# Kernel optimization log

Hardware: AMD Instinct MI355X
Metric: run time of the kernel (lower is better)

The kernel has to match this reference:

```python
import jax, jax.numpy as jnp
import numpy as np

B, N, E = 32, 116, 1346
IN_V, IN_E, H, OUT = 116, 5, 64, 4
NEG_SLOPE = 0.01  # torch LeakyReLU default


def setup_inputs() -> dict:
    key = jax.random.key(0)
    ks = jax.random.split(key, 13)
    return {
        "H_v": jax.random.normal(ks[0], (B * N, IN_V), jnp.float32),
        "H_e": jax.random.normal(ks[1], (B * E, IN_E), jnp.float32),
        "adj_v": jax.random.uniform(ks[2], (B * N, N), jnp.float32),
        "adj_e": jax.random.uniform(ks[3], (B * E, E), jnp.float32),
        "T": jax.random.uniform(ks[4], (B * N, E), jnp.float32),
        "W_v": jax.random.normal(ks[5], (IN_V, H), jnp.float32) * (1.0 / np.sqrt(H)),
        "p_v": jax.random.normal(ks[6], (1, IN_E), jnp.float32),
        "b_v": jax.random.normal(ks[7], (H,), jnp.float32) * 0.01,
        "W_e": jax.random.normal(ks[8], (IN_E, H), jnp.float32) * (1.0 / np.sqrt(H)),
        "p_e": jax.random.normal(ks[9], (1, H), jnp.float32),
        "b_e": jax.random.normal(ks[10], (H,), jnp.float32) * 0.01,
        "W_fc": jax.random.normal(ks[11], (H, OUT), jnp.float32) * (1.0 / np.sqrt(OUT)),
        "b_fc": jax.random.normal(ks[12], (OUT,), jnp.float32) * 0.01,
    }


def _net(H_v, H_e, adj_v, adj_e, T, W_v, p_v, b_v, W_e, p_e, b_e, W_fc, b_fc):
    # reshape flat [B*N, ...] / [B*E, ...] layouts to batched, as in AlternateConvolution.forward
    Hv = H_v.reshape(B, N, IN_V)
    He = H_e.reshape(B, E, IN_E)
    Av = adj_v.reshape(B, N, N)
    Ae = adj_e.reshape(B, E, E)
    Tm = T.reshape(B, N, E)
    eyeN = jnp.eye(N, dtype=bool)
    eyeE = jnp.eye(E, dtype=bool)

    # ---- node layer (AlternateConvolution, node_layer=True) ----
    de = jnp.einsum('bef,f->be', He, p_v[0])                      # H_e @ p^T -> diag values [B,E]
    mult1 = jnp.einsum('bne,be,bme->bnm', Tm, de, Tm)             # T diag(de) T^T
    M1 = jnp.where(eyeN, 1.0, mult1)                              # ones on diagonal
    adjA = M1 * Av
    Hv = jnp.einsum('bnm,bmh->bnh', adjA, Hv @ W_v) + b_v         # [B,N,H]
    Hv = jax.nn.leaky_relu(Hv, NEG_SLOPE)

    # ---- edge layer (AlternateConvolution, node_layer=False) ----
    dv = jnp.einsum('bnh,h->bn', Hv, p_e[0])                      # H_v @ p^T -> diag values [B,N]
    mult2 = jnp.einsum('bne,bn,bnf->bef', Tm, dv, Tm)             # T^T diag(dv) T
    M3 = jnp.where(eyeE, 1.0, mult2)
    adjE = M3 * Ae
    adjE = adjE / (jnp.max(adjE, axis=2, keepdims=True) + 1e-10)  # row-max normalize
    He = jnp.einsum('bef,bfh->beh', adjE, He @ W_e) + b_e         # [B,E,H]
    He = jax.nn.leaky_relu(He, NEG_SLOPE)

    # ---- mean graph pooling over nodes + classifier head (dropout off in eval) ----
    pooled = Hv.mean(axis=1)                                      # [B,H]
    return pooled @ W_fc + b_fc                                   # [B,OUT]


def reference(H_v, H_e, adj_v, adj_e, T, W_v, p_v, b_v, W_e, p_e, b_e, W_fc, b_fc):
    return _net(H_v, H_e, adj_v, adj_e, T, W_v, p_v, b_v, W_e, p_e, b_e, W_fc, b_fc)
```

## Files before the change

kernel.cpp:

```cpp
#include <hip/hip_runtime.h>

#define BATCH 32
#define NN 116
#define EE 1346
#define HH 64
#define SPLITS 8
#define ECH 170
#define MBLK 256
#define HVBLK 116
#define GRID1 (MBLK + HVBLK + 1)

typedef __attribute__((ext_vector_type(8))) short bf16x8;
typedef __attribute__((ext_vector_type(4))) float f32x4;

__device__ __forceinline__ unsigned int cvtpk(float a, float b) {
    unsigned int r;
    asm("v_cvt_pk_bf16_f32 %0, %1, %2" : "=v"(r) : "v"(a), "v"(b));
    return r;
}
__device__ __forceinline__ unsigned short bf16_1(float a) {
    union { float f; unsigned int u; } ua; ua.f = a;
    return (unsigned short)((ua.u + 0x7FFFu + ((ua.u >> 16) & 1u)) >> 16);
}
__device__ __forceinline__ float bf2f(unsigned int bits16) {
    union { unsigned int u; float f; } x; x.u = bits16 << 16;
    return x.f;
}

__global__ __launch_bounds__(512) void stage1_kernel(
    const float* __restrict__ T, const float* __restrict__ He,
    const float* __restrict__ pv,
    const float* __restrict__ Hv, const float* __restrict__ Wv,
    const float* __restrict__ bfc,
    unsigned short* __restrict__ part16, float* __restrict__ HvW,
    float* __restrict__ out)
{
    const int blk = blockIdx.x;
    const int tid = threadIdx.x;

    __shared__ float del[192];
    __shared__ unsigned int Tt[128 * 32];
    __shared__ unsigned int dTt[128 * 32];

    if (blk < MBLK) {
        const int s = blk & 7, b = blk >> 3;
        const int e0 = s * ECH;
        const int cnt = min(ECH, EE - e0);
        const int nsteps = 3;

        {
            const float p0 = pv[0], p1 = pv[1], p2 = pv[2], p3 = pv[3], p4 = pv[4];
            for (int i = tid; i < 192; i += 512) {
                float v = 0.f;
                if (i < cnt) {
                    const float* he = He + (size_t)(b * EE + e0 + i) * 5;
                    v = he[0]*p0 + he[1]*p1 + he[2]*p2 + he[3]*p3 + he[4]*p4;
                }
                del[i] = v;
            }
        }

        const int srow = tid >> 2;
        const int q    = tid & 3;
        const bool rowok = srow < NN;
        const float* Trow = T + ((size_t)b * NN + srow) * EE + e0;

        float2 pf[8];
        auto pref_fast = [&](int c) {
            const int k0 = c * 64 + q * 16;
            #pragma unroll
            for (int j = 0; j < 8; ++j) {
                float2 v = {0.f, 0.f};
                if (rowok) v = *(const float2*)&Trow[k0 + 2 * j];
                pf[j] = v;
            }
        };
        auto pref_chk = [&](int c) {
            const int k0 = c * 64 + q * 16;
            #pragma unroll
            for (int j = 0; j < 8; ++j) {
                float2 v = {0.f, 0.f};
                const int k = k0 + 2 * j;
                if (rowok && k + 1 < cnt) v = *(const float2*)&Trow[k];
                else if (rowok && k < cnt) v.x = Trow[k];
                pf[j] = v;
            }
        };
        auto wlds = [&](int c) {
            const int k0 = c * 64 + q * 16;
            uint4 t0, t1, d0, d1;
            unsigned int* tp0 = &t0.x;  unsigned int* tp1 = &t1.x;
            unsigned int* dp0 = &d0.x;  unsigned int* dp1 = &d1.x;
            #pragma unroll
            for (int j = 0; j < 4; ++j) {
                const float2 va = pf[j];
                const float2 vb = pf[4 + j];
                const float2 da = *(const float2*)&del[k0 + 2 * j];
                const float2 db = *(const float2*)&del[k0 + 8 + 2 * j];
                tp0[j] = cvtpk(va.x, va.y);
                tp1[j] = cvtpk(vb.x, vb.y);
                dp0[j] = cvtpk(va.x * da.x, va.y * da.y);
                dp1[j] = cvtpk(vb.x * db.x, vb.y * db.y);
            }
            const int swz = (srow & 7) << 4;
            const int bo  = srow * 128 + q * 32;
            *(uint4*)((char*)Tt  + ((bo) ^ swz))      = t0;
            *(uint4*)((char*)Tt  + ((bo + 16) ^ swz)) = t1;
            *(uint4*)((char*)dTt + ((bo) ^ swz))      = d0;
            *(uint4*)((char*)dTt + ((bo + 16) ^ swz)) = d1;
        };

        const int w = tid >> 6, lane = tid & 63;
        const int wr = w >> 2, wc = w & 3;
        const int rl = lane & 15, g = lane >> 4;

        auto fragT = [&](const unsigned int* base, int row, int kkb) -> bf16x8 {
            return *(const bf16x8*)((const char*)base + ((row * 128 + kkb + g * 16) ^ ((row & 7) << 4)));
        };

        f32x4 acc[4][2] = {};

        pref_fast(0);
        __syncthreads();

        for (int c = 0; c < nsteps; ++c) {
            wlds(c);
            if (c + 1 == nsteps - 1) pref_fast(c + 1);
            else if (c + 1 < nsteps)  pref_chk(c + 1);
            __syncthreads();
            #pragma unroll
            for (int kk = 0; kk < 2; ++kk) {
                bf16x8 af[4], bf[2];
                #pragma unroll
                for (int i = 0; i < 4; ++i) af[i] = fragT(dTt, wr * 64 + i * 16 + rl, kk * 64);
                #pragma unroll
                for (int j = 0; j < 2; ++j) bf[j] = fragT(Tt,  wc * 32 + j * 16 + rl, kk * 64);
                #pragma unroll
                for (int tn = 0; tn < 4; ++tn)
                    #pragma unroll
                    for (int tm = 0; tm < 2; ++tm)
                        acc[tn][tm] = __builtin_amdgcn_mfma_f32_16x16x32_bf16(
                            af[tn], bf[tm], acc[tn][tm], 0, 0, 0);
            }
            __syncthreads();
        }

        #pragma unroll
        for (int tn = 0; tn < 4; ++tn) {
            #pragma unroll
            for (int r = 0; r < 4; ++r) {
                const int grow = wr * 64 + tn * 16 + g * 4 + r;
                if (grow >= NN) continue;
                unsigned short* rowp = part16 + (((size_t)b * NN + grow) * SPLITS + s) * 128;
                #pragma unroll
                for (int tm = 0; tm < 2; ++tm)
                    rowp[wc * 32 + tm * 16 + rl] = bf16_1(acc[tn][tm][r]);
            }
        }
    } else if (blk < MBLK + HVBLK) {
        const int l0 = (blk - MBLK) * 32 + (tid >> 6) * 4;
        const int h  = tid & 63;
        const float* hv0 = Hv + (size_t)(l0 + 0) * NN;
        const float* hv1 = Hv + (size_t)(l0 + 1) * NN;
        const float* hv2 = Hv + (size_t)(l0 + 2) * NN;
        const float* hv3 = Hv + (size_t)(l0 + 3) * NN;
        float a0 = 0.f, a1 = 0.f, a2 = 0.f, a3 = 0.f;
        #pragma unroll 4
        for (int k = 0; k < NN; ++k) {
            const float wv = Wv[k * HH + h];
            a0 = fmaf(hv0[k], wv, a0);
            a1 = fmaf(hv1[k], wv, a1);
            a2 = fmaf(hv2[k], wv, a2);
            a3 = fmaf(hv3[k], wv, a3);
        }
        HvW[(size_t)(l0 + 0) * HH + h] = a0;
        HvW[(size_t)(l0 + 1) * HH + h] = a1;
        HvW[(size_t)(l0 + 2) * HH + h] = a2;
        HvW[(size_t)(l0 + 3) * HH + h] = a3;
    } else {
        if (tid < BATCH * 4) out[tid] = bfc[tid & 3];
    }
}

__global__ __launch_bounds__(256) void stage2_kernel(
    const unsigned short* __restrict__ part16, const float* __restrict__ Av,
    const float* __restrict__ HvW, const float* __restrict__ bv,
    const float* __restrict__ Wfc, float* __restrict__ out)
{
    const int blk = blockIdx.x;
    const int b = blk >> 3;
    const int n0 = (blk & 7) * 16;
    const int tid = threadIdx.x;
    const int w = tid >> 6, lane = tid & 63;
    const int rl = lane & 15, g = lane >> 4;

    __shared__ unsigned int Cb[4096];
    __shared__ unsigned int Ab[1024];
    __shared__ float sl[64];

    for (int idx = tid; idx < 64 * 64; idx += 256) {
        const int h = idx & 63, np = idx >> 6;
        const int n = 2 * np;
        const float v0 = (n < NN)     ? HvW[((size_t)b * NN + n) * HH + h]     : 0.f;
        const float v1 = (n + 1 < NN) ? HvW[((size_t)b * NN + n + 1) * HH + h] : 0.f;
        *(unsigned int*)((char*)Cb + ((h * 256 + np * 4) ^ ((h & 7) << 4))) = cvtpk(v0, v1);
    }

    {
        const int r = tid >> 4, m0 = (tid & 15) * 8;
        const int n = n0 + r;
        float ms[8] = {0.f,0.f,0.f,0.f,0.f,0.f,0.f,0.f};
        unsigned int outw[4];
        if (n < NN) {
            const unsigned short* pp = part16 + (((size_t)b * NN + n) * SPLITS) * 128 + m0;
            #pragma unroll
            for (int s = 0; s < SPLITS; ++s) {
                const uint4 u = *(const uint4*)(pp + (size_t)s * 128);
                const unsigned int* up = &u.x;
                #pragma unroll
                for (int j = 0; j < 4; ++j) {
                    ms[2*j]   += bf2f(up[j] & 0xffffu);
                    ms[2*j+1] += bf2f(up[j] >> 16);
                }
            }
            const float* avp = Av + ((size_t)b * NN + n) * NN;
            #pragma unroll
            for (int j = 0; j < 4; ++j) {
                const int m = m0 + 2 * j;
                const float a0 = (m < NN)     ? avp[m]     : 0.f;
                const float a1 = (m + 1 < NN) ? avp[m + 1] : 0.f;
                const float v0 = a0 * ((m     == n) ? 1.0f : ms[2*j]);
                const float v1 = a1 * ((m + 1 == n) ? 1.0f : ms[2*j+1]);
                outw[j] = cvtpk(v0, v1);
            }
        } else {
            outw[0] = outw[1] = outw[2] = outw[3] = 0u;
        }
        *(uint4*)((char*)Ab + ((r * 256 + m0 * 2) ^ ((r & 7) << 4))) = *(uint4*)outw;
    }
    __syncthreads();

    f32x4 acc = {};
    #pragma unroll
    for (int kk = 0; kk < 4; ++kk) {
        const int hrow = w * 16 + rl;
        const bf16x8 a  = *(const bf16x8*)((const char*)Ab +
                          ((rl * 256 + kk * 64 + g * 16) ^ ((rl & 7) << 4)));
        const bf16x8 bb = *(const bf16x8*)((const char*)Cb +
                          ((hrow * 256 + kk * 64 + g * 16) ^ ((hrow & 7) << 4)));
        acc = __builtin_amdgcn_mfma_f32_16x16x32_bf16(a, bb, acc, 0, 0, 0);
    }
    {
        const int h = w * 16 + rl;
        const float bias = bv[h];
        float s = 0.f;
        #pragma unroll
        for (int r = 0; r < 4; ++r) {
            const int n = n0 + g * 4 + r;
            if (n < NN) {
                const float x = acc[r] + bias;
                s += (x >= 0.f) ? x : 0.01f * x;
            }
        }
        s += __shfl_xor(s, 16);
        s += __shfl_xor(s, 32);
        if (g == 0) sl[h] = s;
    }
    __syncthreads();

    if (tid < 4) {
        float a = 0.f;
        #pragma unroll 16
        for (int k = 0; k < HH; ++k)
            a = fmaf(sl[k], Wfc[k * 4 + tid], a);
        atomicAdd(&out[b * 4 + tid], a * (1.0f / NN));
    }
}

extern "C" void kernel_launch(void* const* d_in, const int* in_sizes, int n_in,
                              void* d_out, int out_size, void* d_ws, size_t ws_size,
                              hipStream_t stream) {
    const float* Hv  = (const float*)d_in[0];
    const float* He  = (const float*)d_in[1];
    const float* Av  = (const float*)d_in[2];
    const float* T_  = (const float*)d_in[4];
    const float* Wv  = (const float*)d_in[5];
    const float* pv  = (const float*)d_in[6];
    const float* bv  = (const float*)d_in[7];
    const float* Wfc = (const float*)d_in[11];
    const float* bfc = (const float*)d_in[12];
    float* out = (float*)d_out;

    unsigned short* part16 = (unsigned short*)d_ws;
    float* HvW = (float*)(part16 + (size_t)BATCH * NN * SPLITS * 128);

    stage1_kernel<<<GRID1, 512, 0, stream>>>(
        T_, He, pv, Hv, Wv, bfc, part16, HvW, out);
    stage2_kernel<<<BATCH * 8, 256, 0, stream>>>(
        part16, Av, HvW, bv, Wfc, out);
}
```

Before: 31.95 us.

## Prefetch all T chunks up front and fold HvW GEMV into MFMA blocks

New measurement: 38.78 us. 1.21x slower.

```diff
diff --git a/kernel.cpp b/kernel.cpp
--- a/kernel.cpp
+++ b/kernel.cpp
@@ -7,8 +7,6 @@
 #define SPLITS 8
 #define ECH 170
 #define MBLK 256
-#define HVBLK 116
-#define GRID1 (MBLK + HVBLK + 1)
 
 typedef __attribute__((ext_vector_type(8))) short bf16x8;
 typedef __attribute__((ext_vector_type(4))) float f32x4;
@@ -37,64 +35,63 @@
 {
     const int blk = blockIdx.x;
     const int tid = threadIdx.x;
+    const int s = blk & 7, b = blk >> 3;
+    const int e0 = s * ECH;
+    const int cnt = min(ECH, EE - e0);
 
     __shared__ float del[192];
-    __shared__ unsigned int Tt[128 * 32];
-    __shared__ unsigned int dTt[128 * 32];
-
-    if (blk < MBLK) {
-        const int s = blk & 7, b = blk >> 3;
-        const int e0 = s * ECH;
-        const int cnt = min(ECH, EE - e0);
-        const int nsteps = 3;
-
-        {
-            const float p0 = pv[0], p1 = pv[1], p2 = pv[2], p3 = pv[3], p4 = pv[4];
-            for (int i = tid; i < 192; i += 512) {
-                float v = 0.f;
-                if (i < cnt) {
-                    const float* he = He + (size_t)(b * EE + e0 + i) * 5;
-                    v = he[0]*p0 + he[1]*p1 + he[2]*p2 + he[3]*p3 + he[4]*p4;
-                }
-                del[i] = v;
-            }
-        }
-
-        const int srow = tid >> 2;
-        const int q    = tid & 3;
-        const bool rowok = srow < NN;
-        const float* Trow = T + ((size_t)b * NN + srow) * EE + e0;
-
-        float2 pf[8];
-        auto pref_fast = [&](int c) {
-            const int k0 = c * 64 + q * 16;
-            #pragma unroll
-            for (int j = 0; j < 8; ++j) {
-                float2 v = {0.f, 0.f};
-                if (rowok) v = *(const float2*)&Trow[k0 + 2 * j];
-                pf[j] = v;
-            }
-        };
-        auto pref_chk = [&](int c) {
-            const int k0 = c * 64 + q * 16;
-            #pragma unroll
-            for (int j = 0; j < 8; ++j) {
-                float2 v = {0.f, 0.f};
-                const int k = k0 + 2 * j;
+    __shared__ unsigned int Tt[3 * 128 * 32];
+    __shared__ unsigned int dTt[3 * 128 * 32];
+
+    if (blk == 0 && tid < BATCH * 4) out[tid] = bfc[tid & 3];
+
+    const int srow = tid >> 2;
+    const int q    = tid & 3;
+    const bool rowok = srow < NN;
+    const float* Trow = T + ((size_t)b * NN + srow) * EE + e0;
+
+    float2 pf[24];
+    #pragma unroll
+    for (int c = 0; c < 3; ++c) {
+        #pragma unroll
+        for (int j = 0; j < 8; ++j) {
+            const int k = c * 64 + q * 16 + 2 * j;
+            float2 v = {0.f, 0.f};
+            if (c < 2) {
+                if (rowok) v = *(const float2*)&Trow[k];
+            } else {
                 if (rowok && k + 1 < cnt) v = *(const float2*)&Trow[k];
                 else if (rowok && k < cnt) v.x = Trow[k];
-                pf[j] = v;
-            }
-        };
-        auto wlds = [&](int c) {
+            }
+            pf[c * 8 + j] = v;
+        }
+    }
+
+    {
+        const float p0 = pv[0], p1 = pv[1], p2 = pv[2], p3 = pv[3], p4 = pv[4];
+        for (int i = tid; i < 192; i += 512) {
+            float v = 0.f;
+            if (i < cnt) {
+                const float* he = He + (size_t)(b * EE + e0 + i) * 5;
+                v = he[0]*p0 + he[1]*p1 + he[2]*p2 + he[3]*p3 + he[4]*p4;
+            }
+            del[i] = v;
+        }
+    }
+    __syncthreads();
+
+    {
+        const int swz = (srow & 7) << 4;
+        #pragma unroll
+        for (int c = 0; c < 3; ++c) {
             const int k0 = c * 64 + q * 16;
             uint4 t0, t1, d0, d1;
             unsigned int* tp0 = &t0.x;  unsigned int* tp1 = &t1.x;
             unsigned int* dp0 = &d0.x;  unsigned int* dp1 = &d1.x;
             #pragma unroll
             for (int j = 0; j < 4; ++j) {
-                const float2 va = pf[j];
-                const float2 vb = pf[4 + j];
+                const float2 va = pf[c * 8 + j];
+                const float2 vb = pf[c * 8 + 4 + j];
                 const float2 da = *(const float2*)&del[k0 + 2 * j];
                 const float2 db = *(const float2*)&del[k0 + 8 + 2 * j];
                 tp0[j] = cvtpk(va.x, va.y);
@@ -102,83 +99,71 @@
                 dp0[j] = cvtpk(va.x * da.x, va.y * da.y);
                 dp1[j] = cvtpk(vb.x * db.x, vb.y * db.y);
             }
-            const int swz = (srow & 7) << 4;
-            const int bo  = srow * 128 + q * 32;
-            *(uint4*)((char*)Tt  + ((bo) ^ swz))      = t0;
-            *(uint4*)((char*)Tt  + ((bo + 16) ^ swz)) = t1;
-            *(uint4*)((char*)dTt + ((bo) ^ swz))      = d0;
-            *(uint4*)((char*)dTt + ((bo + 16) ^ swz)) = d1;
-        };
-
-        const int w = tid >> 6, lane = tid & 63;
-        const int wr = w >> 2, wc = w & 3;
-        const int rl = lane & 15, g = lane >> 4;
-
-        auto fragT = [&](const unsigned int* base, int row, int kkb) -> bf16x8 {
-            return *(const bf16x8*)((const char*)base + ((row * 128 + kkb + g * 16) ^ ((row & 7) << 4)));
-        };
-
-        f32x4 acc[4][2] = {};
-
-        pref_fast(0);
-        __syncthreads();
-
-        for (int c = 0; c < nsteps; ++c) {
-            wlds(c);
-            if (c + 1 == nsteps - 1) pref_fast(c + 1);
-            else if (c + 1 < nsteps)  pref_chk(c + 1);
-            __syncthreads();
-            #pragma unroll
-            for (int kk = 0; kk < 2; ++kk) {
-                bf16x8 af[4], bf[2];
-                #pragma unroll
-                for (int i = 0; i < 4; ++i) af[i] = fragT(dTt, wr * 64 + i * 16 + rl, kk * 64);
-                #pragma unroll
-                for (int j = 0; j < 2; ++j) bf[j] = fragT(Tt,  wc * 32 + j * 16 + rl, kk * 64);
-                #pragma unroll
-                for (int tn = 0; tn < 4; ++tn)
-                    #pragma unroll
-                    for (int tm = 0; tm < 2; ++tm)
-                        acc[tn][tm] = __builtin_amdgcn_mfma_f32_16x16x32_bf16(
-                            af[tn], bf[tm], acc[tn][tm], 0, 0, 0);
-            }
-            __syncthreads();
-        }
-
-        #pragma unroll
-        for (int tn = 0; tn < 4; ++tn) {
-            #pragma unroll
-            for (int r = 0; r < 4; ++r) {
-                const int grow = wr * 64 + tn * 16 + g * 4 + r;
-                if (grow >= NN) continue;
-                unsigned short* rowp = part16 + (((size_t)b * NN + grow) * SPLITS + s) * 128;
+            const int bo = c * 16384 + srow * 128 + q * 32;
+            *(uint4*)((char*)Tt  + (c * 16384 + ((srow * 128 + q * 32)      ^ swz))) = t0;
+            *(uint4*)((char*)Tt  + (c * 16384 + ((srow * 128 + q * 32 + 16) ^ swz))) = t1;
+            *(uint4*)((char*)dTt + (c * 16384 + ((srow * 128 + q * 32)      ^ swz))) = d0;
+            *(uint4*)((char*)dTt + (c * 16384 + ((srow * 128 + q * 32 + 16) ^ swz))) = d1;
+            (void)bo;
+        }
+    }
+    __syncthreads();
+
+    const int w = tid >> 6, lane = tid & 63;
+    const int wr = w >> 2, wc = w & 3;
+    const int rl = lane & 15, g = lane >> 4;
+
+    auto fragT = [&](const unsigned int* base, int c, int row, int kkb) -> bf16x8 {
+        return *(const bf16x8*)((const char*)base +
+               (c * 16384 + ((row * 128 + kkb + g * 16) ^ ((row & 7) << 4))));
+    };
+
+    f32x4 acc[4][2] = {};
+    #pragma unroll
+    for (int c = 0; c < 3; ++c) {
+        #pragma unroll
+        for (int kk = 0; kk < 2; ++kk) {
+            bf16x8 af[4], bf[2];
+            #pragma unroll
+            for (int i = 0; i < 4; ++i) af[i] = fragT(dTt, c, wr * 64 + i * 16 + rl, kk * 64);
+            #pragma unroll
+            for (int j = 0; j < 2; ++j) bf[j] = fragT(Tt,  c, wc * 32 + j * 16 + rl, kk * 64);
+            #pragma unroll
+            for (int tn = 0; tn < 4; ++tn)
                 #pragma unroll
                 for (int tm = 0; tm < 2; ++tm)
-                    rowp[wc * 32 + tm * 16 + rl] = bf16_1(acc[tn][tm][r]);
-            }
-        }
-    } else if (blk < MBLK + HVBLK) {
-        const int l0 = (blk - MBLK) * 32 + (tid >> 6) * 4;
-        const int h  = tid & 63;
-        const float* hv0 = Hv + (size_t)(l0 + 0) * NN;
-        const float* hv1 = Hv + (size_t)(l0 + 1) * NN;
-        const float* hv2 = Hv + (size_t)(l0 + 2) * NN;
-        const float* hv3 = Hv + (size_t)(l0 + 3) * NN;
-        float a0 = 0.f, a1 = 0.f, a2 = 0.f, a3 = 0.f;
-        #pragma unroll 4
-        for (int k = 0; k < NN; ++k) {
-            const float wv = Wv[k * HH + h];
-            a0 = fmaf(hv0[k], wv, a0);
-            a1 = fmaf(hv1[k], wv, a1);
-            a2 = fmaf(hv2[k], wv, a2);
-            a3 = fmaf(hv3[k], wv, a3);
-        }
-        HvW[(size_t)(l0 + 0) * HH + h] = a0;
-        HvW[(size_t)(l0 + 1) * HH + h] = a1;
-        HvW[(size_t)(l0 + 2) * HH + h] = a2;
-        HvW[(size_t)(l0 + 3) * HH + h] = a3;
-    } else {
-        if (tid < BATCH * 4) out[tid] = bfc[tid & 3];
+                    acc[tn][tm] = __builtin_amdgcn_mfma_f32_16x16x32_bf16(
+                        af[tn], bf[tm], acc[tn][tm], 0, 0, 0);
+        }
+    }
+
+    #pragma unroll
+    for (int tn = 0; tn < 4; ++tn) {
+        #pragma unroll
+        for (int r = 0; r < 4; ++r) {
+            const int grow = wr * 64 + tn * 16 + g * 4 + r;
+            if (grow >= NN) continue;
+            unsigned short* rowp = part16 + (((size_t)b * NN + grow) * SPLITS + s) * 128;
+            #pragma unroll
+            for (int tm = 0; tm < 2; ++tm)
+                rowp[wc * 32 + tm * 16 + rl] = bf16_1(acc[tn][tm][r]);
+        }
+    }
+
+    {
+        const int h = tid & 63;
+        const int ridx = tid >> 6;
+        const int rbase = s * 15;
+        const int nrows = min(15, NN - rbase);
+        for (int rr = ridx; rr < nrows; rr += 8) {
+            const int n = rbase + rr;
+            const float* hv = Hv + ((size_t)b * NN + n) * NN;
+            float a = 0.f;
+            #pragma unroll 4
+            for (int k = 0; k < NN; ++k)
+                a = fmaf(hv[k], Wv[k * HH + h], a);
+            HvW[((size_t)b * NN + n) * HH + h] = a;
+        }
     }
 }
 
@@ -294,7 +279,7 @@
     unsigned short* part16 = (unsigned short*)d_ws;
     float* HvW = (float*)(part16 + (size_t)BATCH * NN * SPLITS * 128);
 
-    stage1_kernel<<<GRID1, 512, 0, stream>>>(
+    stage1_kernel<<<MBLK, 512, 0, stream>>>(
         T_, He, pv, Hv, Wv, bfc, part16, HvW, out);
     stage2_kernel<<<BATCH * 8, 256, 0, stream>>>(
         part16, Av, HvW, bv, Wfc, out);
```
